# Performance work log

Hardware: AMD Instinct MI355X
Metric: run time of the kernel (lower is better)

The kernel has to match this reference:

```python
import jax, jax.numpy as jnp
import numpy as np

# BlendParams defaults (pytorch3d)
SIGMA = 1e-4
GAMMA = 1e-4
ZNEAR = 1.0
ZFAR = 100.0
EPS = 1e-10

N, H, W, K, C = 4, 256, 256, 8, 16
V, F = 100000, 200000


def setup_inputs() -> dict:
    key = jax.random.key(0)
    ks = jax.random.split(key, 7)
    return {
        "dists": jax.random.normal(ks[0], (N, H, W, K), dtype=jnp.float32),
        "zbuf": jax.random.uniform(ks[1], (N, H, W, K), dtype=jnp.float32),
        "bary_coords": jax.random.uniform(ks[2], (N, H, W, K, 3), dtype=jnp.float32),
        "verts_features": jax.random.normal(ks[3], (V, C), dtype=jnp.float32),
        "background": jax.random.uniform(ks[4], (C,), dtype=jnp.float32),
        "pix_to_face": jax.random.randint(ks[5], (N, H, W, K), 0, F),
        "faces": jax.random.randint(ks[6], (F, 3), 0, V),
    }


def reference(dists, zbuf, bary_coords, verts_features, background, pix_to_face, faces):
    mask = (pix_to_face >= 0)
    maskf = mask.astype(dists.dtype)
    safe_idx = jnp.where(mask, pix_to_face, 0)

    # --- sample_textures (TexturesVertex): barycentric gather ---
    # faces[safe_idx]: (N,H,W,K,3) vertex ids -> (N,H,W,K,3,C) features
    face_vert_feats = verts_features[faces[safe_idx]]
    texels = jnp.einsum("nhwkv,nhwkvc->nhwkc", bary_coords, face_vert_feats)

    # --- softmax_blend ---
    prob_map = jax.nn.sigmoid(-dists / SIGMA) * maskf                 # (N,H,W,K)
    z_inv = (ZFAR - zbuf) / (ZFAR - ZNEAR) * maskf                    # (N,H,W,K)
    z_inv_max = jnp.clip(jnp.max(z_inv, axis=-1, keepdims=True), EPS)  # (N,H,W,1)
    weights_num = prob_map * jnp.exp((z_inv - z_inv_max) / GAMMA)      # (N,H,W,K)
    delta = jnp.clip(jnp.exp((EPS - z_inv_max) / GAMMA), EPS)          # (N,H,W,1)
    denom = jnp.sum(weights_num, axis=-1, keepdims=True) + delta       # (N,H,W,1)

    weighted_colors = jnp.einsum("nhwk,nhwkc->nhwc", weights_num, texels)
    pixel_colors = (weighted_colors + delta * background) / denom      # (N,H,W,C)
    return pixel_colors
```

## Files before the change

### kernel.cpp

```cpp
#include <hip/hip_runtime.h>


constexpr int KK = 8;
constexpr int CC = 16;

__global__ __launch_bounds__(256) void feature_shader(
    const float* __restrict__ dists,
    const float* __restrict__ zbuf,
    const float* __restrict__ bary,
    const float* __restrict__ vfeat,
    const float* __restrict__ bg,
    const int*   __restrict__ p2f,
    const int*   __restrict__ faces,
    float* __restrict__ out,
    int npix)
{
    const float INV_SIGMA = 1e4f;
    const float INV_GAMMA = 1e4f;
    const float EPS       = 1e-10f;
    const float ZFAR      = 100.f;
    const float INV_SPAN  = 1.f / 99.f;

    int p = blockIdx.x * blockDim.x + threadIdx.x;
    if (p >= npix) return;

    const float4* z4 = (const float4*)(zbuf  + (size_t)p * KK);
    const float4* d4 = (const float4*)(dists + (size_t)p * KK);
    const int4*   f4 = (const int4*)  (p2f   + (size_t)p * KK);
    float4 za = z4[0], zb = z4[1];
    float4 da = d4[0], db = d4[1];
    int4   fa = f4[0], fb = f4[1];

    float z[8] = {za.x, za.y, za.z, za.w, zb.x, zb.y, zb.z, zb.w};
    float d[8] = {da.x, da.y, da.z, da.w, db.x, db.y, db.z, db.w};
    int   f[8] = {fa.x, fa.y, fa.z, fa.w, fb.x, fb.y, fb.z, fb.w};

    float zinv[8];
    float m = EPS;
    #pragma unroll
    for (int k = 0; k < 8; ++k) {
        float v = (f[k] >= 0) ? (ZFAR - z[k]) * INV_SPAN : 0.f;
        zinv[k] = v;
        m = fmaxf(m, v);
    }

    float delta = fmaxf(__expf((EPS - m) * INV_GAMMA), EPS);

    float w[8];
    float denom = delta;
    #pragma unroll
    for (int k = 0; k < 8; ++k) {
        float e    = __expf((zinv[k] - m) * INV_GAMMA);
        float prob = (f[k] >= 0) ? (1.f / (1.f + __expf(d[k] * INV_SIGMA))) : 0.f;
        float wk   = prob * e;
        w[k] = wk;
        denom += wk;
    }
    float thr = denom * 1e-7f;

    float acc[16];
    #pragma unroll
    for (int c = 0; c < 16; ++c) acc[c] = 0.f;

    #pragma unroll
    for (int k = 0; k < 8; ++k) {
        if (w[k] > thr) {
            int idx = f[k];
            int v0 = faces[idx * 3 + 0];
            int v1 = faces[idx * 3 + 1];
            int v2 = faces[idx * 3 + 2];
            const float* bp = bary + (size_t)(p * KK + k) * 3;
            float b0 = bp[0] * w[k];
            float b1 = bp[1] * w[k];
            float b2 = bp[2] * w[k];
            const float4* t0 = (const float4*)(vfeat + (size_t)v0 * CC);
            const float4* t1 = (const float4*)(vfeat + (size_t)v1 * CC);
            const float4* t2 = (const float4*)(vfeat + (size_t)v2 * CC);
            #pragma unroll
            for (int j = 0; j < 4; ++j) {
                float4 a0 = t0[j], a1 = t1[j], a2 = t2[j];
                acc[j * 4 + 0] += b0 * a0.x + b1 * a1.x + b2 * a2.x;
                acc[j * 4 + 1] += b0 * a0.y + b1 * a1.y + b2 * a2.y;
                acc[j * 4 + 2] += b0 * a0.z + b1 * a1.z + b2 * a2.z;
                acc[j * 4 + 3] += b0 * a0.w + b1 * a1.w + b2 * a2.w;
            }
        }
    }

    float inv_den = 1.f / denom;
    float4* out4 = (float4*)(out + (size_t)p * CC);
    const float4* bg4 = (const float4*)bg;
    #pragma unroll
    for (int j = 0; j < 4; ++j) {
        float4 g = bg4[j];
        float4 o;
        o.x = (acc[j * 4 + 0] + delta * g.x) * inv_den;
        o.y = (acc[j * 4 + 1] + delta * g.y) * inv_den;
        o.z = (acc[j * 4 + 2] + delta * g.z) * inv_den;
        o.w = (acc[j * 4 + 3] + delta * g.w) * inv_den;
        out4[j] = o;
    }
}

extern "C" void kernel_launch(void* const* d_in, const int* in_sizes, int n_in,
                              void* d_out, int out_size, void* d_ws, size_t ws_size,
                              hipStream_t stream) {
    const float* dists = (const float*)d_in[0];
    const float* zbuf  = (const float*)d_in[1];
    const float* bary  = (const float*)d_in[2];
    const float* vfeat = (const float*)d_in[3];
    const float* bg    = (const float*)d_in[4];
    const int*   p2f   = (const int*)d_in[5];
    const int*   faces = (const int*)d_in[6];
    float* out = (float*)d_out;

    int npix = in_sizes[0] / KK;
    int block = 256;
    int grid = (npix + block - 1) / block;

    hipLaunchKernelGGL(feature_shader, dim3(grid), dim3(block), 0, stream,
                       dists, zbuf, bary, vfeat, bg, p2f, faces, out, npix);
}
```

Baseline: 121.1 us.

## Map one thread per (pixel, K) sample with shuffle reductions across lanes

Work is reassigned from one thread per pixel to one thread per (pixel, k) sample, with eight lanes cooperating on each pixel. The max and sum over K become xor-shuffle reductions, and the 16-channel accumulator is reduced with a recursive-halving shuffle so each lane writes two output channels. This aims to expose 8x more threads so the scattered face and vertex-feature gathers are issued in parallel, hiding gather latency and giving coalesced input loads and output stores. In exchange it adds shuffle traffic and redundant per-lane computation of delta and denom.

```diff
diff --git a/kernel.cpp b/kernel.cpp
--- a/kernel.cpp
+++ b/kernel.cpp
@@ -13,7 +13,7 @@
     const int*   __restrict__ p2f,
     const int*   __restrict__ faces,
     float* __restrict__ out,
-    int npix)
+    int n)
 {
     const float INV_SIGMA = 1e4f;
     const float INV_GAMMA = 1e4f;
@@ -21,85 +21,99 @@
     const float ZFAR      = 100.f;
     const float INV_SPAN  = 1.f / 99.f;
 
-    int p = blockIdx.x * blockDim.x + threadIdx.x;
-    if (p >= npix) return;
+    int t = blockIdx.x * blockDim.x + threadIdx.x;
+    if (t >= n) return;
+    int k = t & (KK - 1);
 
-    const float4* z4 = (const float4*)(zbuf  + (size_t)p * KK);
-    const float4* d4 = (const float4*)(dists + (size_t)p * KK);
-    const int4*   f4 = (const int4*)  (p2f   + (size_t)p * KK);
-    float4 za = z4[0], zb = z4[1];
-    float4 da = d4[0], db = d4[1];
-    int4   fa = f4[0], fb = f4[1];
+    float z  = zbuf[t];
+    float dd = dists[t];
+    int   f  = p2f[t];
 
-    float z[8] = {za.x, za.y, za.z, za.w, zb.x, zb.y, zb.z, zb.w};
-    float d[8] = {da.x, da.y, da.z, da.w, db.x, db.y, db.z, db.w};
-    int   f[8] = {fa.x, fa.y, fa.z, fa.w, fb.x, fb.y, fb.z, fb.w};
+    float zinv = (f >= 0) ? (ZFAR - z) * INV_SPAN : 0.f;
 
-    float zinv[8];
-    float m = EPS;
-    #pragma unroll
-    for (int k = 0; k < 8; ++k) {
-        float v = (f[k] >= 0) ? (ZFAR - z[k]) * INV_SPAN : 0.f;
-        zinv[k] = v;
-        m = fmaxf(m, v);
-    }
+    float m = zinv;
+    m = fmaxf(m, __shfl_xor(m, 1));
+    m = fmaxf(m, __shfl_xor(m, 2));
+    m = fmaxf(m, __shfl_xor(m, 4));
+    m = fmaxf(m, EPS);
 
     float delta = fmaxf(__expf((EPS - m) * INV_GAMMA), EPS);
+    float prob  = (f >= 0) ? 1.f / (1.f + __expf(dd * INV_SIGMA)) : 0.f;
+    float w     = prob * __expf((zinv - m) * INV_GAMMA);
 
-    float w[8];
-    float denom = delta;
-    #pragma unroll
-    for (int k = 0; k < 8; ++k) {
-        float e    = __expf((zinv[k] - m) * INV_GAMMA);
-        float prob = (f[k] >= 0) ? (1.f / (1.f + __expf(d[k] * INV_SIGMA))) : 0.f;
-        float wk   = prob * e;
-        w[k] = wk;
-        denom += wk;
-    }
+    float denom = w;
+    denom += __shfl_xor(denom, 1);
+    denom += __shfl_xor(denom, 2);
+    denom += __shfl_xor(denom, 4);
+    denom += delta;
     float thr = denom * 1e-7f;
 
-    float acc[16];
+    float acc[CC];
     #pragma unroll
-    for (int c = 0; c < 16; ++c) acc[c] = 0.f;
+    for (int c = 0; c < CC; ++c) acc[c] = 0.f;
 
-    #pragma unroll
-    for (int k = 0; k < 8; ++k) {
-        if (w[k] > thr) {
-            int idx = f[k];
-            int v0 = faces[idx * 3 + 0];
-            int v1 = faces[idx * 3 + 1];
-            int v2 = faces[idx * 3 + 2];
-            const float* bp = bary + (size_t)(p * KK + k) * 3;
-            float b0 = bp[0] * w[k];
-            float b1 = bp[1] * w[k];
-            float b2 = bp[2] * w[k];
-            const float4* t0 = (const float4*)(vfeat + (size_t)v0 * CC);
-            const float4* t1 = (const float4*)(vfeat + (size_t)v1 * CC);
-            const float4* t2 = (const float4*)(vfeat + (size_t)v2 * CC);
-            #pragma unroll
-            for (int j = 0; j < 4; ++j) {
-                float4 a0 = t0[j], a1 = t1[j], a2 = t2[j];
-                acc[j * 4 + 0] += b0 * a0.x + b1 * a1.x + b2 * a2.x;
-                acc[j * 4 + 1] += b0 * a0.y + b1 * a1.y + b2 * a2.y;
-                acc[j * 4 + 2] += b0 * a0.z + b1 * a1.z + b2 * a2.z;
-                acc[j * 4 + 3] += b0 * a0.w + b1 * a1.w + b2 * a2.w;
-            }
+    if (w > thr) {
+        int v0 = faces[f * 3 + 0];
+        int v1 = faces[f * 3 + 1];
+        int v2 = faces[f * 3 + 2];
+        const float* bp = bary + (size_t)t * 3;
+        float b0 = bp[0] * w, b1 = bp[1] * w, b2 = bp[2] * w;
+        const float4* t0 = (const float4*)(vfeat + (size_t)v0 * CC);
+        const float4* t1 = (const float4*)(vfeat + (size_t)v1 * CC);
+        const float4* t2 = (const float4*)(vfeat + (size_t)v2 * CC);
+        #pragma unroll
+        for (int j = 0; j < 4; ++j) {
+            float4 a0 = t0[j], a1 = t1[j], a2 = t2[j];
+            acc[j * 4 + 0] = b0 * a0.x + b1 * a1.x + b2 * a2.x;
+            acc[j * 4 + 1] = b0 * a0.y + b1 * a1.y + b2 * a2.y;
+            acc[j * 4 + 2] = b0 * a0.z + b1 * a1.z + b2 * a2.z;
+            acc[j * 4 + 3] = b0 * a0.w + b1 * a1.w + b2 * a2.w;
         }
     }
 
+    {
+        bool low = (k & 4) == 0;
+        float nxt[8];
+        #pragma unroll
+        for (int i = 0; i < 8; ++i) {
+            float send = low ? acc[8 + i] : acc[i];
+            float recv = __shfl_xor(send, 4);
+            nxt[i] = (low ? acc[i] : acc[8 + i]) + recv;
+        }
+        #pragma unroll
+        for (int i = 0; i < 8; ++i) acc[i] = nxt[i];
+    }
+    {
+        bool low = (k & 2) == 0;
+        float nxt[4];
+        #pragma unroll
+        for (int i = 0; i < 4; ++i) {
+            float send = low ? acc[4 + i] : acc[i];
+            float recv = __shfl_xor(send, 2);
+            nxt[i] = (low ? acc[i] : acc[4 + i]) + recv;
+        }
+        #pragma unroll
+        for (int i = 0; i < 4; ++i) acc[i] = nxt[i];
+    }
+    {
+        bool low = (k & 1) == 0;
+        float nxt[2];
+        #pragma unroll
+        for (int i = 0; i < 2; ++i) {
+            float send = low ? acc[2 + i] : acc[i];
+            float recv = __shfl_xor(send, 1);
+            nxt[i] = (low ? acc[i] : acc[2 + i]) + recv;
+        }
+        acc[0] = nxt[0];
+        acc[1] = nxt[1];
+    }
+
+    float2 g = ((const float2*)bg)[k];
     float inv_den = 1.f / denom;
-    float4* out4 = (float4*)(out + (size_t)p * CC);
-    const float4* bg4 = (const float4*)bg;
-    #pragma unroll
-    for (int j = 0; j < 4; ++j) {
-        float4 g = bg4[j];
-        float4 o;
-        o.x = (acc[j * 4 + 0] + delta * g.x) * inv_den;
-        o.y = (acc[j * 4 + 1] + delta * g.y) * inv_den;
-        o.z = (acc[j * 4 + 2] + delta * g.z) * inv_den;
-        o.w = (acc[j * 4 + 3] + delta * g.w) * inv_den;
-        out4[j] = o;
-    }
+    float2 o;
+    o.x = (acc[0] + delta * g.x) * inv_den;
+    o.y = (acc[1] + delta * g.y) * inv_den;
+    ((float2*)out)[t] = o;
 }
 
 extern "C" void kernel_launch(void* const* d_in, const int* in_sizes, int n_in,
@@ -114,10 +128,10 @@
     const int*   faces = (const int*)d_in[6];
     float* out = (float*)d_out;
 
-    int npix = in_sizes[0] / KK;
+    int n = in_sizes[0];
     int block = 256;
-    int grid = (npix + block - 1) / block;
+    int grid = (n + block - 1) / block;
 
     hipLaunchKernelGGL(feature_shader, dim3(grid), dim3(block), 0, stream,
-                       dists, zbuf, bary, vfeat, bg, p2f, faces, out, npix);
+                       dists, zbuf, bary, vfeat, bg, p2f, faces, out, n);
 }
```

Result: no change. 120.5 us (-0.5%).
